# Optimization experiments

Measured on AMD Instinct MI355X. Metric: run time of the kernel, lower is better.

The kernel has to match this reference:

```python
import jax, jax.numpy as jnp
import numpy as np

# Dims: N tokens, top_k K, E experts, d_model D, expert hidden H
N, K, E, D, H = 4096, 2, 8, 1024, 1024


def setup_inputs() -> dict:
    key = jax.random.key(0)
    k1, k2, k3, k4, k5, k6 = jax.random.split(key, 6)
    x = jax.random.normal(k1, (N, D), dtype=jnp.float32)
    expert_indices = jax.random.randint(k2, (N, K), 0, E, dtype=jnp.int32)
    ew = jax.random.uniform(k3, (N, K), dtype=jnp.float32)
    expert_weights = ew / ew.sum(-1, keepdims=True)  # router probs over top-k
    # histogram consistent with expert_indices (computed by the router in the real model)
    batch_size_per_expert = jnp.bincount(expert_indices.reshape(-1), length=E).astype(jnp.int32)
    w1 = jax.random.normal(k4, (E, D, H), dtype=jnp.float32) * (D ** -0.5)
    w3 = jax.random.normal(k5, (E, D, H), dtype=jnp.float32) * (D ** -0.5)
    w2 = jax.random.normal(k6, (E, H, D), dtype=jnp.float32) * (H ** -0.5)
    return {
        "x": x,
        "expert_weights": expert_weights,
        "expert_indices": expert_indices,
        "batch_size_per_expert": batch_size_per_expert,
        "w1": w1,
        "w2": w2,
        "w3": w3,
    }


def reference(x, expert_weights, expert_indices, batch_size_per_expert, w1, w2, w3):
    """Dropless MoE: sort token-copies by expert, grouped-GEMM SwiGLU, unpermute+combine."""
    nk = N * K
    flat_idx = expert_indices.reshape(nk)               # (N*K,)
    order = jnp.argsort(flat_idx)                        # stable sort -> permutation into expert order
    x_perm = x[order // K]                               # (N*K, D) gather source token per copy
    gs = batch_size_per_expert.astype(jnp.int32)         # grouped-GEMM group sizes, sums to N*K
    # per-expert SwiGLU MLP via grouped GEMM (rows of x_perm are contiguous per expert)
    h = jax.nn.silu(jax.lax.ragged_dot(x_perm, w1, gs)) * jax.lax.ragged_dot(x_perm, w3, gs)  # (N*K, H)
    out_perm = jax.lax.ragged_dot(h, w2, gs)             # (N*K, D)
    # unpermute: scatter rows back to original (token, k) order
    out_flat = jnp.zeros_like(x_perm).at[order].set(out_perm)  # (N*K, D)
    # weighted combine over top-k copies
    out = jnp.einsum("nk,nkd->nd", expert_weights, out_flat.reshape(N, K, D))
    return out
```

## Files before the change

kernel.cpp:

```cpp
#include <hip/hip_runtime.h>
#include <hip/hip_bf16.h>
#include <stdint.h>

#define N_TOK   4096
#define TOPK    2
#define N_EXP   8
#define D_MODEL 1024
#define H_DIM   1024
#define NK      (N_TOK * TOPK)
#define MAX_TILES 72

typedef __attribute__((ext_vector_type(8))) short bf16x8;
typedef __attribute__((ext_vector_type(4))) float f32x4;
typedef __attribute__((ext_vector_type(4))) unsigned int uint32x4;
typedef __attribute__((ext_vector_type(2))) unsigned int uint32x2;
typedef unsigned short bfbits;

__device__ inline bfbits f2bf_bits(float f) {
  union { float f; unsigned int u; } v; v.f = f;
  unsigned int r = v.u + 0x7FFFu + ((v.u >> 16) & 1u);
  return (bfbits)(r >> 16);
}
__device__ inline float bf2f(unsigned short u) {
  union { unsigned int u; float f; } v; v.u = ((unsigned int)u) << 16;
  return v.f;
}

__device__ inline void glds16(const bfbits* g, bfbits* l) {
  __builtin_amdgcn_global_load_lds(
      (const __attribute__((address_space(1))) void*)g,
      (__attribute__((address_space(3))) void*)l, 16, 0, 0);
}

__global__ __launch_bounds__(256, 4) void prepass_kernel(
    const float* __restrict__ x, const int* __restrict__ eidx,
    const int* __restrict__ bspe,
    const float* __restrict__ w1, const float* __restrict__ w2,
    const float* __restrict__ w3,
    bfbits* __restrict__ w1t, bfbits* __restrict__ w2t,
    bfbits* __restrict__ w3t, bfbits* __restrict__ xb,
    int* __restrict__ meta, int* __restrict__ row_src,
    int* __restrict__ pos_of) {
  int z = blockIdx.z;
  int tid = threadIdx.x;

  if (z >= 1 && z <= 24) {
    int zz = z - 1;
    const size_t MAT = (size_t)1024 * 1024;
    const float* src; bfbits* dst;
    if (zz < 8)       { src = w1 + (size_t)zz * MAT;        dst = w1t + (size_t)zz * MAT; }
    else if (zz < 16) { src = w3 + (size_t)(zz - 8) * MAT;  dst = w3t + (size_t)(zz - 8) * MAT; }
    else              { src = w2 + (size_t)(zz - 16) * MAT; dst = w2t + (size_t)(zz - 16) * MAT; }

    __shared__ __align__(16) bfbits Ts[64 * 132];
    char* tsb = (char*)Ts;

    int r0 = blockIdx.y * 128, c0 = blockIdx.x * 64;
    int k = tid & 15, qw = tid >> 4;
    int c = k * 4;

    float4 v0[4], v1[4];
#pragma unroll
    for (int it = 0; it < 4; it++) {
      int r = it * 32 + qw * 2;
      v0[it] = *(const float4*)&src[(size_t)(r0 + r) * 1024 + c0 + c];
      v1[it] = *(const float4*)&src[(size_t)(r0 + r + 1) * 1024 + c0 + c];
    }
#pragma unroll
    for (int it = 0; it < 4; it++) {
      int r = it * 32 + qw * 2;
      const float* a0 = (const float*)&v0[it];
      const float* a1 = (const float*)&v1[it];
#pragma unroll
      for (int j = 0; j < 4; j++) {
        int a = c + j;
        int xo = ((a >> 4) & 3) << 3;
        unsigned int pk = (unsigned int)f2bf_bits(a0[j]) |
                          ((unsigned int)f2bf_bits(a1[j]) << 16);
        *(unsigned int*)(tsb + a * 264 + ((r * 2) ^ xo)) = pk;
      }
    }
    __syncthreads();
    int g = tid >> 3, m = tid & 7;
#pragma unroll
    for (int it2 = 0; it2 < 2; it2++) {
      int o = it2 * 32 + g;
      int base = o * 264;
      int xo = ((o >> 4) & 3) << 3;
      uint32x2 p0 = *(const uint32x2*)(tsb + base + ((m * 32 +  0) ^ xo));
      uint32x2 p1 = *(const uint32x2*)(tsb + base + ((m * 32 +  8) ^ xo));
      uint32x2 p2 = *(const uint32x2*)(tsb + base + ((m * 32 + 16) ^ xo));
      uint32x2 p3 = *(const uint32x2*)(tsb + base + ((m * 32 + 24) ^ xo));
      size_t ob = (size_t)(c0 + o) * 1024 + r0 + m * 16;
      uint32x4 s0; s0.x = p0.x; s0.y = p0.y; s0.z = p1.x; s0.w = p1.y;
      uint32x4 s1; s1.x = p2.x; s1.y = p2.y; s1.z = p3.x; s1.w = p3.y;
      *(uint32x4*)&dst[ob] = s0;
      *(uint32x4*)&dst[ob + 8] = s1;
    }
  } else if (z >= 25) {
    int idx = (z - 25) * 128 + blockIdx.y * 16 + blockIdx.x;
    const float4* xv = (const float4*)x;
    ushort4* xo = (ushort4*)xb;
#pragma unroll
    for (int q = 0; q < 4; q++) {
      int fi = idx * 1024 + q * 256 + tid;
      float4 v = xv[fi];
      ushort4 o;
      o.x = f2bf_bits(v.x); o.y = f2bf_bits(v.y);
      o.z = f2bf_bits(v.z); o.w = f2bf_bits(v.w);
      xo[fi] = o;
    }
  } else {
    if (blockIdx.x != 0 || blockIdx.y != 0) return;
    __shared__ int sm[162];
    __shared__ int scnt[N_EXP];
    if (tid == 0) {
      int acc = 0, nt = 0;
      for (int e = 0; e < N_EXP; e++) {
        sm[e] = acc;
        int g = bspe[e];
        for (int tt = 0; tt * 128 < g; tt++) {
          sm[18 + nt] = e;
          sm[90 + nt] = acc + tt * 128;
          nt++;
        }
        acc += g;
      }
      sm[8] = acc;
      sm[17] = nt;
      for (int i = nt; i < MAX_TILES; i++) { sm[18 + i] = 0; sm[90 + i] = 0; }
    }
    if (tid < N_EXP) scnt[tid] = 0;
    __syncthreads();
    int4 eb[8];
#pragma unroll
    for (int q = 0; q < 8; q++) eb[q] = ((const int4*)eidx)[q * 256 + tid];
#pragma unroll
    for (int q = 0; q < 8; q++) {
      int ii = (q * 256 + tid) * 4;
      const int* ev = (const int*)&eb[q];
#pragma unroll
      for (int j = 0; j < 4; j++) {
        int e = ev[j];
        int p = sm[e] + atomicAdd(&scnt[e], 1);
        row_src[p] = ii + j;
        pos_of[ii + j] = p;
      }
    }
    if (tid < 162) meta[tid] = sm[tid];
  }
}

__global__ __launch_bounds__(256, 3) void gemm_swiglu_kernel(
    const bfbits* __restrict__ xb, const bfbits* __restrict__ w1t,
    const bfbits* __restrict__ w3t, const int* __restrict__ row_src,
    const int* __restrict__ meta, bfbits* __restrict__ hb) {
  int nt = meta[17];
  int bt = blockIdx.y;
  if (bt >= nt) return;
  int e = meta[18 + bt];
  int row0 = meta[90 + bt];
  int rows_end = meta[e + 1];
  int n0 = blockIdx.x * 64;

  __shared__ __align__(16) bfbits As[128 * 64];
  __shared__ __align__(16) bfbits B1s[64 * 64];
  __shared__ __align__(16) bfbits B3s[64 * 64];

  int tid = threadIdx.x, lane = tid & 63, wv = tid >> 6;
  int r8 = lane >> 3, jl = lane & 7;
  int jg = jl ^ r8;

  const bfbits* gp[8]; bfbits* lp[8];
  for (int j = 0; j < 8; j++) {
    int s = wv * 8 + j;
    if (s < 16) {
      int tok = row_src[row0 + s * 8 + r8] >> 1;
      gp[j] = xb + (size_t)tok * D_MODEL + jg * 8;
      lp[j] = As + s * 512;
    } else if (s < 24) {
      int b = s - 16;
      gp[j] = w1t + ((size_t)e * H_DIM + n0 + b * 8 + r8) * D_MODEL + jg * 8;
      lp[j] = B1s + b * 512;
    } else {
      int b = s - 24;
      gp[j] = w3t + ((size_t)e * H_DIM + n0 + b * 8 + r8) * D_MODEL + jg * 8;
      lp[j] = B3s + b * 512;
    }
  }

  const f32x4 fzero = {0.f, 0.f, 0.f, 0.f};
  f32x4 accg[4][2], accu[4][2];
  for (int i = 0; i < 4; i++)
    for (int j = 0; j < 2; j++) { accg[i][j] = fzero; accu[i][j] = fzero; }

  int mw = (wv & 1) * 64, nwv = (wv >> 1) * 32;
  int qd = lane >> 4, lr = lane & 15, lr7 = lr & 7;

  for (int kk = 0; kk < D_MODEL / 64; kk++) {
    int ko = kk * 64;
    for (int j = 0; j < 8; j++) glds16(gp[j] + ko, lp[j]);
    __syncthreads();
    for (int ks = 0; ks < 2; ks++) {
      int sb = ((ks * 4 + qd) ^ lr7) << 3;
      bf16x8 af[4], b1f[2], b3f[2];
      for (int mi = 0; mi < 4; mi++)
        af[mi] = *(const bf16x8*)&As[(mw + mi * 16 + lr) * 64 + sb];
      for (int ni = 0; ni < 2; ni++) {
        b1f[ni] = *(const bf16x8*)&B1s[(nwv + ni * 16 + lr) * 64 + sb];
        b3f[ni] = *(const bf16x8*)&B3s[(nwv + ni * 16 + lr) * 64 + sb];
      }
      for (int mi = 0; mi < 4; mi++)
        for (int ni = 0; ni < 2; ni++) {
          accg[mi][ni] = __builtin_amdgcn_mfma_f32_16x16x32_bf16(af[mi], b1f[ni], accg[mi][ni], 0, 0, 0);
          accu[mi][ni] = __builtin_amdgcn_mfma_f32_16x16x32_bf16(af[mi], b3f[ni], accu[mi][ni], 0, 0, 0);
        }
    }
    __syncthreads();
  }

  for (int mi = 0; mi < 4; mi++) {
    int rbase = row0 + mw + mi * 16 + qd * 4;
    for (int r = 0; r < 4; r++) {
      int grow = rbase + r;
      if (grow < rows_end) {
        for (int ni = 0; ni < 2; ni++) {
          float gg = accg[mi][ni][r], u = accu[mi][ni][r];
          float h = gg / (1.f + __expf(-gg)) * u;
          hb[(size_t)grow * H_DIM + n0 + nwv + ni * 16 + lr] = f2bf_bits(h);
        }
      }
    }
  }
}

__global__ __launch_bounds__(256, 4) void gemm_out_kernel(
    const bfbits* __restrict__ hb, const bfbits* __restrict__ w2t,
    const int* __restrict__ meta, bfbits* __restrict__ out_perm) {
  int nt = meta[17];
  int bt = blockIdx.y;
  if (bt >= nt) return;
  int e = meta[18 + bt];
  int row0 = meta[90 + bt];
  int rows_end = meta[e + 1];
  int n0 = blockIdx.x * 64;

  __shared__ __align__(16) bfbits As[128 * 64];
  __shared__ __align__(16) bfbits Bs[64 * 64];

  int tid = threadIdx.x, lane = tid & 63, wv = tid >> 6;
  int r8 = lane >> 3, jl = lane & 7;
  int jg = jl ^ r8;

  const bfbits* gp[6]; bfbits* lp[6];
  for (int j = 0; j < 6; j++) {
    int s = wv * 6 + j;
    if (s < 16) {
      gp[j] = hb + (size_t)(row0 + s * 8 + r8) * H_DIM + jg * 8;
      lp[j] = As + s * 512;
    } else {
      int b = s - 16;
      gp[j] = w2t + ((size_t)e * D_MODEL + n0 + b * 8 + r8) * H_DIM + jg * 8;
      lp[j] = Bs + b * 512;
    }
  }

  const f32x4 fzero = {0.f, 0.f, 0.f, 0.f};
  f32x4 acc[4][2];
  for (int i = 0; i < 4; i++)
    for (int j = 0; j < 2; j++) acc[i][j] = fzero;

  int mw = (wv & 1) * 64, nwv = (wv >> 1) * 32;
  int qd = lane >> 4, lr = lane & 15, lr7 = lr & 7;

  for (int kk = 0; kk < H_DIM / 64; kk++) {
    int ko = kk * 64;
    for (int j = 0; j < 6; j++) glds16(gp[j] + ko, lp[j]);
    __syncthreads();
    for (int ks = 0; ks < 2; ks++) {
      int sb = ((ks * 4 + qd) ^ lr7) << 3;
      bf16x8 af[4], bfr[2];
      for (int mi = 0; mi < 4; mi++)
        af[mi] = *(const bf16x8*)&As[(mw + mi * 16 + lr) * 64 + sb];
      for (int ni = 0; ni < 2; ni++)
        bfr[ni] = *(const bf16x8*)&Bs[(nwv + ni * 16 + lr) * 64 + sb];
      for (int mi = 0; mi < 4; mi++)
        for (int ni = 0; ni < 2; ni++)
          acc[mi][ni] = __builtin_amdgcn_mfma_f32_16x16x32_bf16(af[mi], bfr[ni], acc[mi][ni], 0, 0, 0);
    }
    __syncthreads();
  }

  for (int mi = 0; mi < 4; mi++) {
    int rbase = row0 + mw + mi * 16 + qd * 4;
    for (int r = 0; r < 4; r++) {
      int grow = rbase + r;
      if (grow < rows_end) {
        for (int ni = 0; ni < 2; ni++)
          out_perm[(size_t)grow * D_MODEL + n0 + nwv + ni * 16 + lr] = f2bf_bits(acc[mi][ni][r]);
      }
    }
  }
}

__global__ __launch_bounds__(256) void combine_kernel(
    const ushort4* __restrict__ out_perm, const int* __restrict__ pos_of,
    const float* __restrict__ ew, float4* __restrict__ out) {
  int tid = threadIdx.x;
#pragma unroll
  for (int q = 0; q < 4; q++) {
    int i = blockIdx.x * 1024 + q * 256 + tid;
    int tok = i >> 8;
    int col = i & 255;
    int p0 = pos_of[2 * tok], p1 = pos_of[2 * tok + 1];
    float w0 = ew[2 * tok], w1 = ew[2 * tok + 1];
    ushort4 a = out_perm[(size_t)p0 * 256 + col];
    ushort4 b = out_perm[(size_t)p1 * 256 + col];
    float4 o;
    o.x = w0 * bf2f(a.x) + w1 * bf2f(b.x);
    o.y = w0 * bf2f(a.y) + w1 * bf2f(b.y);
    o.z = w0 * bf2f(a.z) + w1 * bf2f(b.z);
    o.w = w0 * bf2f(a.w) + w1 * bf2f(b.w);
    out[i] = o;
  }
}

extern "C" void kernel_launch(void* const* d_in, const int* in_sizes, int n_in,
                              void* d_out, int out_size, void* d_ws, size_t ws_size,
                              hipStream_t stream) {
  const float* x  = (const float*)d_in[0];
  const float* ew = (const float*)d_in[1];
  const int* eidx = (const int*)d_in[2];
  const int* bspe = (const int*)d_in[3];
  const float* w1 = (const float*)d_in[4];
  const float* w2 = (const float*)d_in[5];
  const float* w3 = (const float*)d_in[6];
  float* out = (float*)d_out;

  char* ws = (char*)d_ws;
  const size_t MB = 1024 * 1024;
  bfbits* w1t   = (bfbits*)(ws);
  bfbits* w3t   = (bfbits*)(ws + 16 * MB);
  bfbits* w2t   = (bfbits*)(ws + 32 * MB);
  bfbits* xb    = (bfbits*)(ws + 48 * MB);
  bfbits* hb    = (bfbits*)(ws + 56 * MB);
  bfbits* out_perm = (bfbits*)(ws);
  int* row_src  = (int*)(ws + 72 * MB);
  int* pos_of   = (int*)(ws + 72 * MB + 32 * 1024);
  int* meta     = (int*)(ws + 72 * MB + 64 * 1024);

  prepass_kernel<<<dim3(16, 8, 33), 256, 0, stream>>>(
      x, eidx, bspe, w1, w2, w3, w1t, w2t, w3t, xb, meta, row_src, pos_of);
  gemm_swiglu_kernel<<<dim3(H_DIM / 64, MAX_TILES), 256, 0, stream>>>(
      xb, w1t, w3t, row_src, meta, hb);
  gemm_out_kernel<<<dim3(D_MODEL / 64, MAX_TILES), 256, 0, stream>>>(
      hb, w2t, meta, out_perm);
  combine_kernel<<<(N_TOK * D_MODEL / 4) / 1024, 256, 0, stream>>>(
      (const ushort4*)out_perm, pos_of, ew, (float4*)out);
}
```

Measured before the change: 241.8 us.

## Double-buffer LDS in grouped GEMMs and fuse combine into down-projection via atomics

Both grouped GEMM kernels now stage tiles in two LDS buffers, issuing the next K-slice's global-to-LDS loads before computing on the current one. This removes one barrier per iteration and overlaps memory with MFMA work. Occupancy targets drop to fit the doubled shared memory. The separate combine kernel and the bf16 out_perm buffer are removed: the prepass zeroes the fp32 output, and the down-projection epilogue atomically adds the weighted results straight into token rows. The trade is many scalar float atomics and a nondeterministic summation order.

Measured after the change: 265.1 us. 1.1x slower.

```diff
diff --git a/kernel.cpp b/kernel.cpp
--- a/kernel.cpp
+++ b/kernel.cpp
@@ -40,7 +40,7 @@
     bfbits* __restrict__ w1t, bfbits* __restrict__ w2t,
     bfbits* __restrict__ w3t, bfbits* __restrict__ xb,
     int* __restrict__ meta, int* __restrict__ row_src,
-    int* __restrict__ pos_of) {
+    int* __restrict__ pos_of, float4* __restrict__ outz) {
   int z = blockIdx.z;
   int tid = threadIdx.x;
 
@@ -101,6 +101,7 @@
     int idx = (z - 25) * 128 + blockIdx.y * 16 + blockIdx.x;
     const float4* xv = (const float4*)x;
     ushort4* xo = (ushort4*)xb;
+    const float4 z4 = {0.f, 0.f, 0.f, 0.f};
 #pragma unroll
     for (int q = 0; q < 4; q++) {
       int fi = idx * 1024 + q * 256 + tid;
@@ -109,6 +110,7 @@
       o.x = f2bf_bits(v.x); o.y = f2bf_bits(v.y);
       o.z = f2bf_bits(v.z); o.w = f2bf_bits(v.w);
       xo[fi] = o;
+      outz[fi] = z4;
     }
   } else {
     if (blockIdx.x != 0 || blockIdx.y != 0) return;
@@ -151,7 +153,7 @@
   }
 }
 
-__global__ __launch_bounds__(256, 3) void gemm_swiglu_kernel(
+__global__ __launch_bounds__(256, 2) void gemm_swiglu_kernel(
     const bfbits* __restrict__ xb, const bfbits* __restrict__ w1t,
     const bfbits* __restrict__ w3t, const int* __restrict__ row_src,
     const int* __restrict__ meta, bfbits* __restrict__ hb) {
@@ -163,29 +165,27 @@
   int rows_end = meta[e + 1];
   int n0 = blockIdx.x * 64;
 
-  __shared__ __align__(16) bfbits As[128 * 64];
-  __shared__ __align__(16) bfbits B1s[64 * 64];
-  __shared__ __align__(16) bfbits B3s[64 * 64];
+  __shared__ __align__(16) bfbits smbuf[2][16384];
 
   int tid = threadIdx.x, lane = tid & 63, wv = tid >> 6;
   int r8 = lane >> 3, jl = lane & 7;
   int jg = jl ^ r8;
 
-  const bfbits* gp[8]; bfbits* lp[8];
+  const bfbits* gp[8]; int lpo[8];
   for (int j = 0; j < 8; j++) {
     int s = wv * 8 + j;
     if (s < 16) {
       int tok = row_src[row0 + s * 8 + r8] >> 1;
       gp[j] = xb + (size_t)tok * D_MODEL + jg * 8;
-      lp[j] = As + s * 512;
+      lpo[j] = s * 512;
     } else if (s < 24) {
       int b = s - 16;
       gp[j] = w1t + ((size_t)e * H_DIM + n0 + b * 8 + r8) * D_MODEL + jg * 8;
-      lp[j] = B1s + b * 512;
+      lpo[j] = 8192 + b * 512;
     } else {
       int b = s - 24;
       gp[j] = w3t + ((size_t)e * H_DIM + n0 + b * 8 + r8) * D_MODEL + jg * 8;
-      lp[j] = B3s + b * 512;
+      lpo[j] = 12288 + b * 512;
     }
   }
 
@@ -197,10 +197,19 @@
   int mw = (wv & 1) * 64, nwv = (wv >> 1) * 32;
   int qd = lane >> 4, lr = lane & 15, lr7 = lr & 7;
 
+  for (int j = 0; j < 8; j++) glds16(gp[j], &smbuf[0][0] + lpo[j]);
+  __syncthreads();
+
   for (int kk = 0; kk < D_MODEL / 64; kk++) {
-    int ko = kk * 64;
-    for (int j = 0; j < 8; j++) glds16(gp[j] + ko, lp[j]);
-    __syncthreads();
+    int cur = kk & 1;
+    if (kk < D_MODEL / 64 - 1) {
+      int ko = (kk + 1) * 64;
+      bfbits* nx = &smbuf[cur ^ 1][0];
+      for (int j = 0; j < 8; j++) glds16(gp[j] + ko, nx + lpo[j]);
+    }
+    const bfbits* As  = &smbuf[cur][0];
+    const bfbits* B1s = As + 8192;
+    const bfbits* B3s = As + 12288;
     for (int ks = 0; ks < 2; ks++) {
       int sb = ((ks * 4 + qd) ^ lr7) << 3;
       bf16x8 af[4], b1f[2], b3f[2];
@@ -234,9 +243,10 @@
   }
 }
 
-__global__ __launch_bounds__(256, 4) void gemm_out_kernel(
+__global__ __launch_bounds__(256, 3) void gemm_out_kernel(
     const bfbits* __restrict__ hb, const bfbits* __restrict__ w2t,
-    const int* __restrict__ meta, bfbits* __restrict__ out_perm) {
+    const int* __restrict__ meta, const int* __restrict__ row_src,
+    const float* __restrict__ ew, float* __restrict__ out) {
   int nt = meta[17];
   int bt = blockIdx.y;
   if (bt >= nt) return;
@@ -245,23 +255,22 @@
   int rows_end = meta[e + 1];
   int n0 = blockIdx.x * 64;
 
-  __shared__ __align__(16) bfbits As[128 * 64];
-  __shared__ __align__(16) bfbits Bs[64 * 64];
+  __shared__ __align__(16) bfbits smbuf[2][12288];
 
   int tid = threadIdx.x, lane = tid & 63, wv = tid >> 6;
   int r8 = lane >> 3, jl = lane & 7;
   int jg = jl ^ r8;
 
-  const bfbits* gp[6]; bfbits* lp[6];
+  const bfbits* gp[6]; int lpo[6];
   for (int j = 0; j < 6; j++) {
     int s = wv * 6 + j;
     if (s < 16) {
       gp[j] = hb + (size_t)(row0 + s * 8 + r8) * H_DIM + jg * 8;
-      lp[j] = As + s * 512;
+      lpo[j] = s * 512;
     } else {
       int b = s - 16;
       gp[j] = w2t + ((size_t)e * D_MODEL + n0 + b * 8 + r8) * H_DIM + jg * 8;
-      lp[j] = Bs + b * 512;
+      lpo[j] = 8192 + b * 512;
     }
   }
 
@@ -273,10 +282,18 @@
   int mw = (wv & 1) * 64, nwv = (wv >> 1) * 32;
   int qd = lane >> 4, lr = lane & 15, lr7 = lr & 7;
 
+  for (int j = 0; j < 6; j++) glds16(gp[j], &smbuf[0][0] + lpo[j]);
+  __syncthreads();
+
   for (int kk = 0; kk < H_DIM / 64; kk++) {
-    int ko = kk * 64;
-    for (int j = 0; j < 6; j++) glds16(gp[j] + ko, lp[j]);
-    __syncthreads();
+    int cur = kk & 1;
+    if (kk < H_DIM / 64 - 1) {
+      int ko = (kk + 1) * 64;
+      bfbits* nx = &smbuf[cur ^ 1][0];
+      for (int j = 0; j < 6; j++) glds16(gp[j] + ko, nx + lpo[j]);
+    }
+    const bfbits* As = &smbuf[cur][0];
+    const bfbits* Bs = As + 8192;
     for (int ks = 0; ks < 2; ks++) {
       int sb = ((ks * 4 + qd) ^ lr7) << 3;
       bf16x8 af[4], bfr[2];
@@ -296,32 +313,13 @@
     for (int r = 0; r < 4; r++) {
       int grow = rbase + r;
       if (grow < rows_end) {
+        int src = row_src[grow];
+        float w = ew[src];
+        size_t ob = (size_t)(src >> 1) * D_MODEL + n0 + nwv + lr;
         for (int ni = 0; ni < 2; ni++)
-          out_perm[(size_t)grow * D_MODEL + n0 + nwv + ni * 16 + lr] = f2bf_bits(acc[mi][ni][r]);
-      }
-    }
-  }
-}
-
-__global__ __launch_bounds__(256) void combine_kernel(
-    const ushort4* __restrict__ out_perm, const int* __restrict__ pos_of,
-    const float* __restrict__ ew, float4* __restrict__ out) {
-  int tid = threadIdx.x;
-#pragma unroll
-  for (int q = 0; q < 4; q++) {
-    int i = blockIdx.x * 1024 + q * 256 + tid;
-    int tok = i >> 8;
-    int col = i & 255;
-    int p0 = pos_of[2 * tok], p1 = pos_of[2 * tok + 1];
-    float w0 = ew[2 * tok], w1 = ew[2 * tok + 1];
-    ushort4 a = out_perm[(size_t)p0 * 256 + col];
-    ushort4 b = out_perm[(size_t)p1 * 256 + col];
-    float4 o;
-    o.x = w0 * bf2f(a.x) + w1 * bf2f(b.x);
-    o.y = w0 * bf2f(a.y) + w1 * bf2f(b.y);
-    o.z = w0 * bf2f(a.z) + w1 * bf2f(b.z);
-    o.w = w0 * bf2f(a.w) + w1 * bf2f(b.w);
-    out[i] = o;
+          atomicAdd(&out[ob + ni * 16], w * acc[mi][ni][r]);
+      }
+    }
   }
 }
 
@@ -344,17 +342,15 @@
   bfbits* w2t   = (bfbits*)(ws + 32 * MB);
   bfbits* xb    = (bfbits*)(ws + 48 * MB);
   bfbits* hb    = (bfbits*)(ws + 56 * MB);
-  bfbits* out_perm = (bfbits*)(ws);
   int* row_src  = (int*)(ws + 72 * MB);
   int* pos_of   = (int*)(ws + 72 * MB + 32 * 1024);
   int* meta     = (int*)(ws + 72 * MB + 64 * 1024);
 
   prepass_kernel<<<dim3(16, 8, 33), 256, 0, stream>>>(
-      x, eidx, bspe, w1, w2, w3, w1t, w2t, w3t, xb, meta, row_src, pos_of);
+      x, eidx, bspe, w1, w2, w3, w1t, w2t, w3t, xb, meta, row_src, pos_of,
+      (float4*)out);
   gemm_swiglu_kernel<<<dim3(H_DIM / 64, MAX_TILES), 256, 0, stream>>>(
       xb, w1t, w3t, row_src, meta, hb);
   gemm_out_kernel<<<dim3(D_MODEL / 64, MAX_TILES), 256, 0, stream>>>(
-      hb, w2t, meta, out_perm);
-  combine_kernel<<<(N_TOK * D_MODEL / 4) / 1024, 256, 0, stream>>>(
-      (const ushort4*)out_perm, pos_of, ew, (float4*)out);
-}
+      hb, w2t, meta, row_src, ew, out);
+}
```
